# Optimization experiments

Measured on AMD Instinct MI355X. Metric: run time of the kernel, lower is better.

The kernel has to match this reference:

```python
import jax, jax.numpy as jnp
import numpy as np

IN, OUT, E, R = 2048, 2048, 8, 8

def setup_inputs() -> dict:
    key = jax.random.key(0)
    ks = jax.random.split(key, 8)
    B, S = 4, 2048
    x = jax.random.normal(ks[0], (B, S, IN), dtype=jnp.float32)
    routing_weights = jax.random.uniform(ks[1], (B, E), dtype=jnp.float32)
    W = jax.random.normal(ks[2], (OUT, IN), dtype=jnp.float32) / np.sqrt(IN).astype(np.float32)
    b = jax.random.normal(ks[3], (OUT,), dtype=jnp.float32) * 0.01
    lora_A_s = jax.random.normal(ks[4], (IN, R), dtype=jnp.float32) / np.sqrt(IN).astype(np.float32)
    lora_B_s = jax.random.normal(ks[5], (R, OUT), dtype=jnp.float32) * 0.01
    lora_A_e = jax.random.normal(ks[6], (E, IN, R), dtype=jnp.float32) / np.sqrt(IN).astype(np.float32)
    lora_B_e = jax.random.normal(ks[7], (E, R, OUT), dtype=jnp.float32) * 0.01
    return {"x": x, "routing_weights": routing_weights, "W": W, "b": b,
            "lora_A_s": lora_A_s, "lora_B_s": lora_B_s,
            "lora_A_e": lora_A_e, "lora_B_e": lora_B_e}

def reference(x, routing_weights, W, b, lora_A_s, lora_B_s, lora_A_e, lora_B_e):
    # base linear: [B,S,IN] @ [IN,OUT] + [OUT]
    base_out = jnp.einsum('bsi,oi->bso', x, W) + b
    # shared low-rank path
    shared_out = (x @ lora_A_s) @ lora_B_s
    # all experts batched: t[b,s,e,r] = x @ A_e[e]; weighted reduce over experts
    t = jnp.einsum('bsi,eir->bser', x, lora_A_e)          # [B,S,E,R]
    expert_out = jnp.einsum('bser,ero,be->bso', t, lora_B_e, routing_weights)
    return base_out + shared_out + expert_out
```

## Files before the change

### kernel.cpp

```cpp
#include <hip/hip_runtime.h>
#include <hip/hip_bf16.h>

#define IN_DIM 2048
#define OUT_DIM 2048
#define NE 8
#define M_TOT 8192
#define RANK_PAD 128
#define K_EXT 2176
#define NKT 34

typedef short short8 __attribute__((ext_vector_type(8)));
typedef float floatx4 __attribute__((ext_vector_type(4)));
typedef unsigned short us;

__device__ __forceinline__ us f2bf(float f) {
    __hip_bfloat16 h = __float2bfloat16(f);
    return *reinterpret_cast<us*>(&h);
}

__device__ __forceinline__ void gld_lds16(const void* g, void* l) {
    __builtin_amdgcn_global_load_lds(
        (const __attribute__((address_space(1))) void*)g,
        (__attribute__((address_space(3))) void*)l, 16, 0, 0);
}


__device__ __forceinline__ void stage2(const us* src, char* lds) {
    gld_lds16(src, lds);
    gld_lds16(src + 128 * K_EXT, lds + 8192);
}

__device__ __forceinline__ void mfma_quad(floatx4 (&acc)[8][4], const short8 (&af)[4],
                                          const short8 (&bf)[4], int mq) {
#pragma unroll
    for (int i = 0; i < 4; ++i)
#pragma unroll
        for (int ni = 0; ni < 4; ++ni)
            acc[mq * 4 + i][ni] =
                __builtin_amdgcn_mfma_f32_16x16x32_bf16(af[i], bf[ni], acc[mq * 4 + i][ni], 0, 0, 0);
}

template <int SM, int VM0, int VM2, bool RD3>
__device__ __forceinline__ void ktile(
    const us* __restrict__ pA, const us* __restrict__ pB, int k1, int k2,
    const char* smC, const char* smN, char* lwC, char* lwN,
    int ab, int bb,
    short8 (&afA)[4], short8 (&afB)[4], short8 (&bfA)[4], short8 (&bfB)[4],
    floatx4 (&acc)[8][4])
{
#pragma unroll
    for (int i = 0; i < 4; ++i) afB[i] = *(const short8*)(smC + ab + (4 + i) * 1024);
    asm volatile("s_waitcnt lgkmcnt(4)" ::: "memory");
    __builtin_amdgcn_sched_barrier(0);
    __builtin_amdgcn_s_setprio(1);
    mfma_quad(acc, afA, bfA, 0);
    __builtin_amdgcn_s_setprio(0);
    if (SM & 1) stage2(pA + k1 + 32, lwN + 32768);
    if (VM0 == 8)      asm volatile("s_waitcnt vmcnt(8)" ::: "memory");
    else if (VM0 == 0) asm volatile("s_waitcnt vmcnt(0)" ::: "memory");
    __builtin_amdgcn_s_barrier();

#pragma unroll
    for (int i = 0; i < 4; ++i) afA[i] = *(const short8*)(smC + 32768 + ab + (4 + i) * 1024);
#pragma unroll
    for (int i = 0; i < 4; ++i) bfB[i] = *(const short8*)(smC + 32768 + bb + i * 1024);
    asm volatile("s_waitcnt lgkmcnt(8)" ::: "memory");
    __builtin_amdgcn_sched_barrier(0);
    __builtin_amdgcn_s_setprio(1);
    mfma_quad(acc, afB, bfA, 1);
    __builtin_amdgcn_s_setprio(0);
    if (SM & 2) stage2(pB + k2, lwC + 16384);
    __builtin_amdgcn_s_barrier();

#pragma unroll
    for (int i = 0; i < 4; ++i) afB[i] = *(const short8*)(smC + 32768 + ab + i * 1024);
    asm volatile("s_waitcnt lgkmcnt(4)" ::: "memory");
    __builtin_amdgcn_sched_barrier(0);
    __builtin_amdgcn_s_setprio(1);
    mfma_quad(acc, afA, bfB, 1);
    __builtin_amdgcn_s_setprio(0);
    if (SM & 4) stage2(pA + k2, lwC);
    if (VM2 == 8)      asm volatile("s_waitcnt vmcnt(8)" ::: "memory");
    else if (VM2 == 4) asm volatile("s_waitcnt vmcnt(4)" ::: "memory");
    __builtin_amdgcn_s_barrier();

    if (RD3) {
#pragma unroll
        for (int i = 0; i < 4; ++i) afA[i] = *(const short8*)(smN + ab + i * 1024);
#pragma unroll
        for (int i = 0; i < 4; ++i) bfA[i] = *(const short8*)(smN + bb + i * 1024);
        asm volatile("s_waitcnt lgkmcnt(8)" ::: "memory");
    } else {
        asm volatile("s_waitcnt lgkmcnt(0)" ::: "memory");
    }
    __builtin_amdgcn_sched_barrier(0);
    __builtin_amdgcn_s_setprio(1);
    mfma_quad(acc, afB, bfB, 0);
    __builtin_amdgcn_s_setprio(0);
    if (SM & 8) stage2(pB + k2 + 32, lwC + 49152);
    __builtin_amdgcn_s_barrier();
}

__global__ __launch_bounds__(512) void main_gemm8(const us* __restrict__ A,
                                                  const us* __restrict__ B,
                                                  const float* __restrict__ bias,
                                                  float* __restrict__ out) {
    extern __shared__ char smem[];
    int tid = threadIdx.x;
    int lane = tid & 63, w = tid >> 6;
    int wm = w >> 2, wn = w & 3;
    int rlo = lane & 15, kq = lane >> 4;

    int b = blockIdx.x;
    int bs = (b & 7) * 32 + (b >> 3);
    int m0 = (bs >> 3) * 256, n0 = (bs & 7) * 256;

    int swz = (kq ^ ((rlo >> 1) & 3)) * 16;
    int ab = (wm * 128 + rlo) * 64 + swz;
    int bb = 16384 + (wn * 64 + rlo) * 64 + swz;

    int r0 = tid >> 2;
    int ps = tid & 3;
    int ssw = (ps ^ ((r0 >> 1) & 3)) * 8;
    const us* pA = A + (size_t)(m0 + r0) * K_EXT + ssw;
    const us* pB = B + (size_t)(n0 + r0) * K_EXT + ssw;
    char* lw0 = smem + w * 1024;
    char* lw1 = lw0 + 65536;
    const char* sm0 = smem;
    const char* sm1 = smem + 65536;

    floatx4 acc[8][4];
#pragma unroll
    for (int mi = 0; mi < 8; ++mi)
#pragma unroll
        for (int ni = 0; ni < 4; ++ni) acc[mi][ni] = (floatx4)0.f;

    stage2(pA,      lw0);
    stage2(pB,      lw0 + 16384);
    stage2(pA + 32, lw0 + 32768);
    stage2(pB + 32, lw0 + 49152);
    stage2(pA + 64, lw1);
    stage2(pB + 64, lw1 + 16384);
    stage2(pB + 96, lw1 + 49152);
    asm volatile("s_waitcnt vmcnt(10)" ::: "memory");
    __builtin_amdgcn_s_barrier();

    short8 afA[4], afB[4], bfA[4], bfB[4];
#pragma unroll
    for (int i = 0; i < 4; ++i) afA[i] = *(const short8*)(sm0 + ab + i * 1024);
#pragma unroll
    for (int i = 0; i < 4; ++i) bfA[i] = *(const short8*)(sm0 + bb + i * 1024);

    for (int tt = 0; tt < 16; ++tt) {
        int t0 = tt * 2;
        ktile<0xF, 8, 8, true>(pA, pB, (t0 + 1) * 64, (t0 + 2) * 64,
                               sm0, sm1, lw0, lw1, ab, bb, afA, afB, bfA, bfB, acc);
        ktile<0xF, 8, 8, true>(pA, pB, (t0 + 2) * 64, (t0 + 3) * 64,
                               sm1, sm0, lw1, lw0, ab, bb, afA, afB, bfA, bfB, acc);
    }
    ktile<0x1, 8, 4, true>(pA, pB, 33 * 64, 34 * 64,
                           sm0, sm1, lw0, lw1, ab, bb, afA, afB, bfA, bfB, acc);
    ktile<0x0, 0, -1, false>(pA, pB, 0, 0,
                             sm1, sm0, lw1, lw0, ab, bb, afA, afB, bfA, bfB, acc);

    float bbias[4];
#pragma unroll
    for (int ni = 0; ni < 4; ++ni) bbias[ni] = bias[n0 + wn * 64 + ni * 16 + rlo];
#pragma unroll
    for (int mi = 0; mi < 8; ++mi) {
        int row = m0 + wm * 128 + mi * 16 + kq * 4;
#pragma unroll
        for (int ni = 0; ni < 4; ++ni) {
            int col = n0 + wn * 64 + ni * 16 + rlo;
#pragma unroll
            for (int r = 0; r < 4; ++r)
                out[(size_t)(row + r) * OUT_DIM + col] = acc[mi][ni][r] + bbias[ni];
        }
    }
}

__global__ void prep_wb(const float* __restrict__ W, const float* __restrict__ Bs,
                        const float* __restrict__ Be, const float* __restrict__ As,
                        const float* __restrict__ Ae, us* __restrict__ Bext,
                        us* __restrict__ AcatT) {
    int blk = blockIdx.x;
    int t = threadIdx.x;
    if (blk < OUT_DIM) {
        int n = blk;
        const float4* src = (const float4*)(W + (size_t)n * IN_DIM + t * 8);
        float4 v0 = src[0], v1 = src[1];
        short8 o;
        o[0] = (short)f2bf(v0.x); o[1] = (short)f2bf(v0.y); o[2] = (short)f2bf(v0.z); o[3] = (short)f2bf(v0.w);
        o[4] = (short)f2bf(v1.x); o[5] = (short)f2bf(v1.y); o[6] = (short)f2bf(v1.z); o[7] = (short)f2bf(v1.w);
        *(short8*)(Bext + (size_t)n * K_EXT + t * 8) = o;
        if (t < RANK_PAD) {
            float v = 0.f;
            if (t < 8)       v = Bs[(size_t)t * OUT_DIM + n];
            else if (t < 72) v = Be[(size_t)(t - 8) * OUT_DIM + n];
            Bext[(size_t)n * K_EXT + IN_DIM + t] = f2bf(v);
        }
    } else {
        int kp = blk - OUT_DIM;
        int i0 = t * 8;
        short8 o;
#pragma unroll
        for (int j = 0; j < 8; ++j) {
            int i = i0 + j;
            float v = 0.f;
            if (kp < 8)       v = As[(size_t)i * 8 + kp];
            else if (kp < 72) v = Ae[(size_t)((kp - 8) >> 3) * IN_DIM * 8 + (size_t)i * 8 + ((kp - 8) & 7)];
            o[j] = (short)f2bf(v);
        }
        *(short8*)(AcatT + (size_t)kp * IN_DIM + i0) = o;
    }
}

__global__ __launch_bounds__(512) void tgemm_fused(const float* __restrict__ x,
                                                   us* __restrict__ Aext,
                                                   const us* __restrict__ AcatT,
                                                   const float* __restrict__ routing) {
    __shared__ floatx4 red[8][64][6];
    int tid = threadIdx.x;
    int lane = tid & 63, w = tid >> 6;
    int rlo = lane & 15, kq = lane >> 4;
    int mbase = blockIdx.x * 16;

    floatx4 acc[6];
#pragma unroll
    for (int ni = 0; ni < 6; ++ni) acc[ni] = (floatx4)0.f;

    const float* xrow = x + (size_t)(mbase + rlo) * IN_DIM + w * 256 + kq * 8;
    us* arow = Aext + (size_t)(mbase + rlo) * K_EXT + w * 256 + kq * 8;
    const us* bbase = AcatT + (size_t)rlo * IN_DIM + w * 256 + kq * 8;

#pragma unroll
    for (int kt = 0; kt < 8; ++kt) {
        int k0 = kt * 32;
        float4 v0 = *(const float4*)(xrow + k0);
        float4 v1 = *(const float4*)(xrow + k0 + 4);
        short8 a;
        a[0] = (short)f2bf(v0.x); a[1] = (short)f2bf(v0.y); a[2] = (short)f2bf(v0.z); a[3] = (short)f2bf(v0.w);
        a[4] = (short)f2bf(v1.x); a[5] = (short)f2bf(v1.y); a[6] = (short)f2bf(v1.z); a[7] = (short)f2bf(v1.w);
        *(short8*)(arow + k0) = a;
#pragma unroll
        for (int ni = 0; ni < 6; ++ni) {
            short8 bfr = *(const short8*)(bbase + (size_t)(ni * 16) * IN_DIM + k0);
            acc[ni] = __builtin_amdgcn_mfma_f32_16x16x32_bf16(a, bfr, acc[ni], 0, 0, 0);
        }
    }

#pragma unroll
    for (int ni = 0; ni < 6; ++ni) red[w][lane][ni] = acc[ni];
    __syncthreads();
    if (w == 0) {
#pragma unroll
        for (int ni = 0; ni < 6; ++ni) {
            floatx4 s = red[0][lane][ni];
#pragma unroll
            for (int ww = 1; ww < 8; ++ww) s += red[ww][lane][ni];
            int col = ni * 16 + rlo;
#pragma unroll
            for (int r = 0; r < 4; ++r) {
                int row = mbase + kq * 4 + r;
                float fac = (col < 8) ? 1.f
                          : (col < 72 ? routing[(row >> 11) * NE + ((col - 8) >> 3)] : 0.f);
                Aext[(size_t)row * K_EXT + IN_DIM + col] = f2bf(s[r] * fac);
            }
        }
#pragma unroll
        for (int c = 0; c < 2; ++c) {
            int col = 96 + c * 16 + rlo;
#pragma unroll
            for (int r = 0; r < 4; ++r)
                Aext[(size_t)(mbase + kq * 4 + r) * K_EXT + IN_DIM + col] = 0;
        }
    }
}

extern "C" void kernel_launch(void* const* d_in, const int* in_sizes, int n_in,
                              void* d_out, int out_size, void* d_ws, size_t ws_size,
                              hipStream_t stream) {
    const float* x   = (const float*)d_in[0];
    const float* rw  = (const float*)d_in[1];
    const float* W   = (const float*)d_in[2];
    const float* bv  = (const float*)d_in[3];
    const float* As  = (const float*)d_in[4];
    const float* Bs  = (const float*)d_in[5];
    const float* Ae  = (const float*)d_in[6];
    const float* Be  = (const float*)d_in[7];
    float* out = (float*)d_out;

    size_t offA = 0;
    size_t offB = offA + (size_t)M_TOT * K_EXT * sizeof(us);
    size_t offC = offB + (size_t)OUT_DIM * K_EXT * sizeof(us);
    size_t need = offC + (size_t)96 * IN_DIM * sizeof(us);
    if (ws_size < need) return;

    us* Aext  = (us*)((char*)d_ws + offA);
    us* Bext  = (us*)((char*)d_ws + offB);
    us* AcatT = (us*)((char*)d_ws + offC);

    hipFuncSetAttribute((const void*)main_gemm8,
                        hipFuncAttributeMaxDynamicSharedMemorySize, 131072);

    prep_wb<<<OUT_DIM + 96, 256, 0, stream>>>(W, Bs, Be, As, Ae, Bext, AcatT);
    tgemm_fused<<<M_TOT / 16, 512, 0, stream>>>(x, Aext, AcatT, rw);
    main_gemm8<<<256, 512, 131072, stream>>>(Aext, Bext, bv, out);
}
```

Measured before the change: 114.6 us.

## Fuse prep, low-rank projection and main GEMM into one cooperative kernel

Merges the three kernel launches (weight/activation conversion, the LoRA projection GEMM, and the main bf16 GEMM) into a single cooperative kernel of 256 blocks separated by two grid-wide syncs. This removes launch gaps and tail effects between kernels. The x-to-bf16 conversion moves into the prep phase, so the projection phase rereads bf16 Aext instead of fp32 x, and each block now handles 32 rows instead of 16. In exchange, the prep and projection phases run on only 256 blocks of 512 threads held to the main GEMM's large shared-memory footprint, which limits their parallelism, and the grid syncs add overhead.

Measured after the change: 344.3 us. +200.5%, slower.

```diff
diff --git a/kernel.cpp b/kernel.cpp
--- a/kernel.cpp
+++ b/kernel.cpp
@@ -1,5 +1,8 @@
 #include <hip/hip_runtime.h>
 #include <hip/hip_bf16.h>
+#include <hip/hip_cooperative_groups.h>
+
+namespace cg = cooperative_groups;
 
 #define IN_DIM 2048
 #define OUT_DIM 2048
@@ -7,7 +10,6 @@
 #define M_TOT 8192
 #define RANK_PAD 128
 #define K_EXT 2176
-#define NKT 34
 
 typedef short short8 __attribute__((ext_vector_type(8)));
 typedef float floatx4 __attribute__((ext_vector_type(4)));
@@ -16,6 +18,15 @@
 __device__ __forceinline__ us f2bf(float f) {
     __hip_bfloat16 h = __float2bfloat16(f);
     return *reinterpret_cast<us*>(&h);
+}
+
+__device__ __forceinline__ short8 cvt8(float4 v0, float4 v1) {
+    short8 o;
+    o[0] = (short)f2bf(v0.x); o[1] = (short)f2bf(v0.y);
+    o[2] = (short)f2bf(v0.z); o[3] = (short)f2bf(v0.w);
+    o[4] = (short)f2bf(v1.x); o[5] = (short)f2bf(v1.y);
+    o[6] = (short)f2bf(v1.z); o[7] = (short)f2bf(v1.w);
+    return o;
 }
 
 __device__ __forceinline__ void gld_lds16(const void* g, void* l) {
@@ -101,18 +112,14 @@
     __builtin_amdgcn_s_barrier();
 }
 
-__global__ __launch_bounds__(512) void main_gemm8(const us* __restrict__ A,
-                                                  const us* __restrict__ B,
-                                                  const float* __restrict__ bias,
-                                                  float* __restrict__ out) {
-    extern __shared__ char smem[];
-    int tid = threadIdx.x;
+__device__ void run_main_gemm(char* smem, int tid, int bid,
+                              const us* __restrict__ A, const us* __restrict__ B,
+                              const float* __restrict__ bias, float* __restrict__ out) {
     int lane = tid & 63, w = tid >> 6;
     int wm = w >> 2, wn = w & 3;
     int rlo = lane & 15, kq = lane >> 4;
 
-    int b = blockIdx.x;
-    int bs = (b & 7) * 32 + (b >> 3);
+    int bs = (bid & 7) * 32 + (bid >> 3);
     int m0 = (bs >> 3) * 256, n0 = (bs & 7) * 256;
 
     int swz = (kq ^ ((rlo >> 1) & 3)) * 16;
@@ -179,102 +186,131 @@
     }
 }
 
-__global__ void prep_wb(const float* __restrict__ W, const float* __restrict__ Bs,
-                        const float* __restrict__ Be, const float* __restrict__ As,
-                        const float* __restrict__ Ae, us* __restrict__ Bext,
-                        us* __restrict__ AcatT) {
-    int blk = blockIdx.x;
-    int t = threadIdx.x;
-    if (blk < OUT_DIM) {
-        int n = blk;
-        const float4* src = (const float4*)(W + (size_t)n * IN_DIM + t * 8);
-        float4 v0 = src[0], v1 = src[1];
-        short8 o;
-        o[0] = (short)f2bf(v0.x); o[1] = (short)f2bf(v0.y); o[2] = (short)f2bf(v0.z); o[3] = (short)f2bf(v0.w);
-        o[4] = (short)f2bf(v1.x); o[5] = (short)f2bf(v1.y); o[6] = (short)f2bf(v1.z); o[7] = (short)f2bf(v1.w);
-        *(short8*)(Bext + (size_t)n * K_EXT + t * 8) = o;
-        if (t < RANK_PAD) {
+__global__ __launch_bounds__(512) void fused_all(
+    const float* __restrict__ x, const float* __restrict__ routing,
+    const float* __restrict__ W, const float* __restrict__ bias,
+    const float* __restrict__ As, const float* __restrict__ Bs,
+    const float* __restrict__ Ae, const float* __restrict__ Be,
+    float* __restrict__ out, us* __restrict__ Aext, us* __restrict__ Bext,
+    us* __restrict__ AcatT)
+{
+    extern __shared__ char smem[];
+    int tid = threadIdx.x;
+    int bid = blockIdx.x;
+
+    {
+        int half = tid >> 8;
+        int t = tid & 255;
+        int col = t * 8;
+#pragma unroll 4
+        for (int rr = 0; rr < 16; ++rr) {
+            int row = bid * 32 + rr * 2 + half;
+            const float4* src = (const float4*)(x + (size_t)row * IN_DIM + col);
+            *(short8*)(Aext + (size_t)row * K_EXT + col) = cvt8(src[0], src[1]);
+        }
+#pragma unroll
+        for (int rr = 0; rr < 4; ++rr) {
+            int n = bid * 8 + rr * 2 + half;
+            const float4* src = (const float4*)(W + (size_t)n * IN_DIM + col);
+            *(short8*)(Bext + (size_t)n * K_EXT + col) = cvt8(src[0], src[1]);
+        }
+#pragma unroll
+        for (int it = 0; it < 2; ++it) {
+            int q = it * 512 + tid;
+            int rrow = q >> 7, ccol = q & 127;
+            int n = bid * 8 + rrow;
             float v = 0.f;
-            if (t < 8)       v = Bs[(size_t)t * OUT_DIM + n];
-            else if (t < 72) v = Be[(size_t)(t - 8) * OUT_DIM + n];
-            Bext[(size_t)n * K_EXT + IN_DIM + t] = f2bf(v);
-        }
-    } else {
-        int kp = blk - OUT_DIM;
-        int i0 = t * 8;
-        short8 o;
-#pragma unroll
-        for (int j = 0; j < 8; ++j) {
-            int i = i0 + j;
-            float v = 0.f;
-            if (kp < 8)       v = As[(size_t)i * 8 + kp];
-            else if (kp < 72) v = Ae[(size_t)((kp - 8) >> 3) * IN_DIM * 8 + (size_t)i * 8 + ((kp - 8) & 7)];
-            o[j] = (short)f2bf(v);
-        }
-        *(short8*)(AcatT + (size_t)kp * IN_DIM + i0) = o;
-    }
-}
-
-__global__ __launch_bounds__(512) void tgemm_fused(const float* __restrict__ x,
-                                                   us* __restrict__ Aext,
-                                                   const us* __restrict__ AcatT,
-                                                   const float* __restrict__ routing) {
-    __shared__ floatx4 red[8][64][6];
-    int tid = threadIdx.x;
-    int lane = tid & 63, w = tid >> 6;
-    int rlo = lane & 15, kq = lane >> 4;
-    int mbase = blockIdx.x * 16;
-
-    floatx4 acc[6];
-#pragma unroll
-    for (int ni = 0; ni < 6; ++ni) acc[ni] = (floatx4)0.f;
-
-    const float* xrow = x + (size_t)(mbase + rlo) * IN_DIM + w * 256 + kq * 8;
-    us* arow = Aext + (size_t)(mbase + rlo) * K_EXT + w * 256 + kq * 8;
-    const us* bbase = AcatT + (size_t)rlo * IN_DIM + w * 256 + kq * 8;
-
-#pragma unroll
-    for (int kt = 0; kt < 8; ++kt) {
-        int k0 = kt * 32;
-        float4 v0 = *(const float4*)(xrow + k0);
-        float4 v1 = *(const float4*)(xrow + k0 + 4);
-        short8 a;
-        a[0] = (short)f2bf(v0.x); a[1] = (short)f2bf(v0.y); a[2] = (short)f2bf(v0.z); a[3] = (short)f2bf(v0.w);
-        a[4] = (short)f2bf(v1.x); a[5] = (short)f2bf(v1.y); a[6] = (short)f2bf(v1.z); a[7] = (short)f2bf(v1.w);
-        *(short8*)(arow + k0) = a;
-#pragma unroll
-        for (int ni = 0; ni < 6; ++ni) {
-            short8 bfr = *(const short8*)(bbase + (size_t)(ni * 16) * IN_DIM + k0);
-            acc[ni] = __builtin_amdgcn_mfma_f32_16x16x32_bf16(a, bfr, acc[ni], 0, 0, 0);
-        }
-    }
-
-#pragma unroll
-    for (int ni = 0; ni < 6; ++ni) red[w][lane][ni] = acc[ni];
-    __syncthreads();
-    if (w == 0) {
-#pragma unroll
-        for (int ni = 0; ni < 6; ++ni) {
-            floatx4 s = red[0][lane][ni];
-#pragma unroll
-            for (int ww = 1; ww < 8; ++ww) s += red[ww][lane][ni];
-            int col = ni * 16 + rlo;
-#pragma unroll
-            for (int r = 0; r < 4; ++r) {
-                int row = mbase + kq * 4 + r;
-                float fac = (col < 8) ? 1.f
-                          : (col < 72 ? routing[(row >> 11) * NE + ((col - 8) >> 3)] : 0.f);
-                Aext[(size_t)row * K_EXT + IN_DIM + col] = f2bf(s[r] * fac);
+            if (ccol < 8)       v = Bs[(size_t)ccol * OUT_DIM + n];
+            else if (ccol < 72) v = Be[(size_t)(ccol - 8) * OUT_DIM + n];
+            Bext[(size_t)n * K_EXT + IN_DIM + ccol] = f2bf(v);
+        }
+        if (bid < 96) {
+            int kp = bid;
+            int i0 = tid * 4;
+#pragma unroll
+            for (int j = 0; j < 4; ++j) {
+                int i = i0 + j;
+                float v = 0.f;
+                if (kp < 8)       v = As[(size_t)i * 8 + kp];
+                else if (kp < 72) v = Ae[(size_t)(kp - 8) + (size_t)i * 8
+                                         + (size_t)((kp - 8) >> 3) * (IN_DIM * 8 - 8)
+                                         + (size_t)0];
+                AcatT[(size_t)kp * IN_DIM + i] = f2bf(v);
             }
         }
-#pragma unroll
-        for (int c = 0; c < 2; ++c) {
-            int col = 96 + c * 16 + rlo;
-#pragma unroll
-            for (int r = 0; r < 4; ++r)
-                Aext[(size_t)(mbase + kq * 4 + r) * K_EXT + IN_DIM + col] = 0;
-        }
-    }
+    }
+
+    cg::grid_group grid = cg::this_grid();
+    __threadfence();
+    grid.sync();
+    __threadfence();
+
+    {
+        floatx4* red = (floatx4*)smem;
+        int lane = tid & 63, w = tid >> 6;
+        int rlo = lane & 15, kq = lane >> 4;
+        int mbase = bid * 32;
+
+        floatx4 acc[2][6];
+#pragma unroll
+        for (int rg = 0; rg < 2; ++rg)
+#pragma unroll
+            for (int ni = 0; ni < 6; ++ni) acc[rg][ni] = (floatx4)0.f;
+
+        const us* a0p = Aext + (size_t)(mbase + rlo) * K_EXT + w * 256 + kq * 8;
+        const us* a1p = Aext + (size_t)(mbase + 16 + rlo) * K_EXT + w * 256 + kq * 8;
+        const us* b0p = AcatT + (size_t)rlo * IN_DIM + w * 256 + kq * 8;
+
+#pragma unroll
+        for (int kt = 0; kt < 8; ++kt) {
+            int k0 = kt * 32;
+            short8 a0 = *(const short8*)(a0p + k0);
+            short8 a1 = *(const short8*)(a1p + k0);
+#pragma unroll
+            for (int ni = 0; ni < 6; ++ni) {
+                short8 bfr = *(const short8*)(b0p + (size_t)(ni * 16) * IN_DIM + k0);
+                acc[0][ni] = __builtin_amdgcn_mfma_f32_16x16x32_bf16(a0, bfr, acc[0][ni], 0, 0, 0);
+                acc[1][ni] = __builtin_amdgcn_mfma_f32_16x16x32_bf16(a1, bfr, acc[1][ni], 0, 0, 0);
+            }
+        }
+#pragma unroll
+        for (int rg = 0; rg < 2; ++rg)
+#pragma unroll
+            for (int ni = 0; ni < 6; ++ni)
+                red[(w * 64 + lane) * 12 + rg * 6 + ni] = acc[rg][ni];
+        __syncthreads();
+        if (w < 2) {
+            int rg = w;
+#pragma unroll
+            for (int ni = 0; ni < 6; ++ni) {
+                floatx4 s = red[lane * 12 + rg * 6 + ni];
+#pragma unroll
+                for (int ww = 1; ww < 8; ++ww)
+                    s += red[(ww * 64 + lane) * 12 + rg * 6 + ni];
+                int col = ni * 16 + rlo;
+#pragma unroll
+                for (int r = 0; r < 4; ++r) {
+                    int row = mbase + rg * 16 + kq * 4 + r;
+                    float fac = (col < 8) ? 1.f
+                              : (col < 72 ? routing[(row >> 11) * NE + ((col - 8) >> 3)] : 0.f);
+                    Aext[(size_t)row * K_EXT + IN_DIM + col] = f2bf(s[r] * fac);
+                }
+            }
+#pragma unroll
+            for (int c = 0; c < 2; ++c) {
+                int col = 96 + c * 16 + rlo;
+#pragma unroll
+                for (int r = 0; r < 4; ++r)
+                    Aext[(size_t)(mbase + rg * 16 + kq * 4 + r) * K_EXT + IN_DIM + col] = 0;
+            }
+        }
+    }
+
+    __threadfence();
+    grid.sync();
+    __threadfence();
+
+    run_main_gemm(smem, tid, bid, Aext, Bext, bias, out);
 }
 
 extern "C" void kernel_launch(void* const* d_in, const int* in_sizes, int n_in,
@@ -300,10 +336,12 @@
     us* Bext  = (us*)((char*)d_ws + offB);
     us* AcatT = (us*)((char*)d_ws + offC);
 
-    hipFuncSetAttribute((const void*)main_gemm8,
+    hipFuncSetAttribute((const void*)fused_all,
                         hipFuncAttributeMaxDynamicSharedMemorySize, 131072);
 
-    prep_wb<<<OUT_DIM + 96, 256, 0, stream>>>(W, Bs, Be, As, Ae, Bext, AcatT);
-    tgemm_fused<<<M_TOT / 16, 512, 0, stream>>>(x, Aext, AcatT, rw);
-    main_gemm8<<<256, 512, 131072, stream>>>(Aext, Bext, bv, out);
-}
+    void* args[] = {(void*)&x, (void*)&rw, (void*)&W, (void*)&bv,
+                    (void*)&As, (void*)&Bs, (void*)&Ae, (void*)&Be,
+                    (void*)&out, (void*)&Aext, (void*)&Bext, (void*)&AcatT};
+    hipLaunchCooperativeKernel((void*)fused_all, dim3(256), dim3(512),
+                               args, 131072, stream);
+}
```

## Merge W-to-bf16 conversion into the x-projection kernel as extra blocks

Applied to the files above, without the earlier changes.

The weight conversion (W and the LoRA B matrices into the extended bf16 B operand) moves out of the first prep kernel and runs as 512 extra blocks of the x-cast/LoRA-A projection kernel. Only the small A-matrix transpose stays in a separate tiny kernel. This lets the weight cast run alongside the activation work and shortens the serial chain of prep launches. The cost is one more small launch and blocks that each carry the large shared-memory reduction buffer even when they do no reduction.

Result: no change. 115.1 us (+0.4%).

```diff
diff --git a/kernel.cpp b/kernel.cpp
--- a/kernel.cpp
+++ b/kernel.cpp
@@ -7,8 +7,8 @@
 #define M_TOT 8192
 #define RANK_PAD 128
 #define K_EXT 2176
-#define NKT 34
-
+
+typedef short short4v __attribute__((ext_vector_type(4)));
 typedef short short8 __attribute__((ext_vector_type(8)));
 typedef float floatx4 __attribute__((ext_vector_type(4)));
 typedef unsigned short us;
@@ -179,51 +179,61 @@
     }
 }
 
-__global__ void prep_wb(const float* __restrict__ W, const float* __restrict__ Bs,
-                        const float* __restrict__ Be, const float* __restrict__ As,
-                        const float* __restrict__ Ae, us* __restrict__ Bext,
-                        us* __restrict__ AcatT) {
-    int blk = blockIdx.x;
-    int t = threadIdx.x;
-    if (blk < OUT_DIM) {
-        int n = blk;
-        const float4* src = (const float4*)(W + (size_t)n * IN_DIM + t * 8);
-        float4 v0 = src[0], v1 = src[1];
-        short8 o;
-        o[0] = (short)f2bf(v0.x); o[1] = (short)f2bf(v0.y); o[2] = (short)f2bf(v0.z); o[3] = (short)f2bf(v0.w);
-        o[4] = (short)f2bf(v1.x); o[5] = (short)f2bf(v1.y); o[6] = (short)f2bf(v1.z); o[7] = (short)f2bf(v1.w);
-        *(short8*)(Bext + (size_t)n * K_EXT + t * 8) = o;
-        if (t < RANK_PAD) {
-            float v = 0.f;
-            if (t < 8)       v = Bs[(size_t)t * OUT_DIM + n];
-            else if (t < 72) v = Be[(size_t)(t - 8) * OUT_DIM + n];
-            Bext[(size_t)n * K_EXT + IN_DIM + t] = f2bf(v);
-        }
-    } else {
-        int kp = blk - OUT_DIM;
-        int i0 = t * 8;
-        short8 o;
-#pragma unroll
-        for (int j = 0; j < 8; ++j) {
-            int i = i0 + j;
-            float v = 0.f;
-            if (kp < 8)       v = As[(size_t)i * 8 + kp];
-            else if (kp < 72) v = Ae[(size_t)((kp - 8) >> 3) * IN_DIM * 8 + (size_t)i * 8 + ((kp - 8) & 7)];
-            o[j] = (short)f2bf(v);
-        }
-        *(short8*)(AcatT + (size_t)kp * IN_DIM + i0) = o;
-    }
-}
-
-__global__ __launch_bounds__(512) void tgemm_fused(const float* __restrict__ x,
-                                                   us* __restrict__ Aext,
-                                                   const us* __restrict__ AcatT,
-                                                   const float* __restrict__ routing) {
+__global__ void prep_acat(const float* __restrict__ As, const float* __restrict__ Ae,
+                          us* __restrict__ AcatT) {
+    int kp = blockIdx.x;
+    int i0 = threadIdx.x * 8;
+    short8 o;
+#pragma unroll
+    for (int j = 0; j < 8; ++j) {
+        int i = i0 + j;
+        float v = 0.f;
+        if (kp < 8)       v = As[(size_t)i * 8 + kp];
+        else if (kp < 72) v = Ae[(size_t)((kp - 8) >> 3) * IN_DIM * 8 + (size_t)i * 8 + ((kp - 8) & 7)];
+        o[j] = (short)f2bf(v);
+    }
+    *(short8*)(AcatT + (size_t)kp * IN_DIM + i0) = o;
+}
+
+__global__ __launch_bounds__(512) void prep_tgemm(
+    const float* __restrict__ x, us* __restrict__ Aext,
+    const us* __restrict__ AcatT, const float* __restrict__ routing,
+    const float* __restrict__ W, const float* __restrict__ Bs,
+    const float* __restrict__ Be, us* __restrict__ Bext)
+{
     __shared__ floatx4 red[8][64][6];
     int tid = threadIdx.x;
+    int bid = blockIdx.x;
+
+    if (bid >= 512) {
+        int base = (bid - 512) * 4;
+        int half = tid >> 8;
+        int t = tid & 255;
+        int col = t * 8;
+#pragma unroll
+        for (int rr = 0; rr < 2; ++rr) {
+            int n = base + rr * 2 + half;
+            const float4* src = (const float4*)(W + (size_t)n * IN_DIM + col);
+            float4 v0 = src[0], v1 = src[1];
+            short8 o;
+            o[0] = (short)f2bf(v0.x); o[1] = (short)f2bf(v0.y);
+            o[2] = (short)f2bf(v0.z); o[3] = (short)f2bf(v0.w);
+            o[4] = (short)f2bf(v1.x); o[5] = (short)f2bf(v1.y);
+            o[6] = (short)f2bf(v1.z); o[7] = (short)f2bf(v1.w);
+            *(short8*)(Bext + (size_t)n * K_EXT + col) = o;
+        }
+        int rrow = tid >> 7, ccol = tid & 127;
+        int n = base + rrow;
+        float v = 0.f;
+        if (ccol < 8)       v = Bs[(size_t)ccol * OUT_DIM + n];
+        else if (ccol < 72) v = Be[(size_t)(ccol - 8) * OUT_DIM + n];
+        Bext[(size_t)n * K_EXT + IN_DIM + ccol] = f2bf(v);
+        return;
+    }
+
     int lane = tid & 63, w = tid >> 6;
     int rlo = lane & 15, kq = lane >> 4;
-    int mbase = blockIdx.x * 16;
+    int mbase = bid * 16;
 
     floatx4 acc[6];
 #pragma unroll
@@ -239,8 +249,10 @@
         float4 v0 = *(const float4*)(xrow + k0);
         float4 v1 = *(const float4*)(xrow + k0 + 4);
         short8 a;
-        a[0] = (short)f2bf(v0.x); a[1] = (short)f2bf(v0.y); a[2] = (short)f2bf(v0.z); a[3] = (short)f2bf(v0.w);
-        a[4] = (short)f2bf(v1.x); a[5] = (short)f2bf(v1.y); a[6] = (short)f2bf(v1.z); a[7] = (short)f2bf(v1.w);
+        a[0] = (short)f2bf(v0.x); a[1] = (short)f2bf(v0.y);
+        a[2] = (short)f2bf(v0.z); a[3] = (short)f2bf(v0.w);
+        a[4] = (short)f2bf(v1.x); a[5] = (short)f2bf(v1.y);
+        a[6] = (short)f2bf(v1.z); a[7] = (short)f2bf(v1.w);
         *(short8*)(arow + k0) = a;
 #pragma unroll
         for (int ni = 0; ni < 6; ++ni) {
@@ -303,7 +315,7 @@
     hipFuncSetAttribute((const void*)main_gemm8,
                         hipFuncAttributeMaxDynamicSharedMemorySize, 131072);
 
-    prep_wb<<<OUT_DIM + 96, 256, 0, stream>>>(W, Bs, Be, As, Ae, Bext, AcatT);
-    tgemm_fused<<<M_TOT / 16, 512, 0, stream>>>(x, Aext, AcatT, rw);
+    prep_acat<<<96, 256, 0, stream>>>(As, Ae, AcatT);
+    prep_tgemm<<<1024, 512, 0, stream>>>(x, Aext, AcatT, rw, W, Bs, Be, Bext);
     main_gemm8<<<256, 512, 131072, stream>>>(Aext, Bext, bv, out);
 }
```

## Move x bf16 conversion into combined streaming prep kernel and read bf16 in tgemm

Applied to the files above, without the earlier changes.

The fp32-to-bf16 conversion of x moves out of the low-rank projection kernel into a single prep kernel that also converts W and builds the LoRA B/A extension tables, with more work per 512-thread block. The projection kernel then reads the already-converted bf16 activations instead of fp32 x. The intent is to decouple bandwidth-bound conversion from the MFMA reduction kernel and make conversion a pure coalesced stream. The cost is an extra read of the bf16 activation buffer in the projection kernel, and the B-extension and A-transpose parts now use narrower scalar stores.

New measurement: 119.4 us. 1.04x slower.

```diff
diff --git a/kernel.cpp b/kernel.cpp
--- a/kernel.cpp
+++ b/kernel.cpp
@@ -7,7 +7,6 @@
 #define M_TOT 8192
 #define RANK_PAD 128
 #define K_EXT 2176
-#define NKT 34
 
 typedef short short8 __attribute__((ext_vector_type(8)));
 typedef float floatx4 __attribute__((ext_vector_type(4)));
@@ -16,6 +15,15 @@
 __device__ __forceinline__ us f2bf(float f) {
     __hip_bfloat16 h = __float2bfloat16(f);
     return *reinterpret_cast<us*>(&h);
+}
+
+__device__ __forceinline__ short8 cvt8(float4 v0, float4 v1) {
+    short8 o;
+    o[0] = (short)f2bf(v0.x); o[1] = (short)f2bf(v0.y);
+    o[2] = (short)f2bf(v0.z); o[3] = (short)f2bf(v0.w);
+    o[4] = (short)f2bf(v1.x); o[5] = (short)f2bf(v1.y);
+    o[6] = (short)f2bf(v1.z); o[7] = (short)f2bf(v1.w);
+    return o;
 }
 
 __device__ __forceinline__ void gld_lds16(const void* g, void* l) {
@@ -179,46 +187,61 @@
     }
 }
 
-__global__ void prep_wb(const float* __restrict__ W, const float* __restrict__ Bs,
-                        const float* __restrict__ Be, const float* __restrict__ As,
-                        const float* __restrict__ Ae, us* __restrict__ Bext,
-                        us* __restrict__ AcatT) {
-    int blk = blockIdx.x;
-    int t = threadIdx.x;
-    if (blk < OUT_DIM) {
-        int n = blk;
-        const float4* src = (const float4*)(W + (size_t)n * IN_DIM + t * 8);
-        float4 v0 = src[0], v1 = src[1];
-        short8 o;
-        o[0] = (short)f2bf(v0.x); o[1] = (short)f2bf(v0.y); o[2] = (short)f2bf(v0.z); o[3] = (short)f2bf(v0.w);
-        o[4] = (short)f2bf(v1.x); o[5] = (short)f2bf(v1.y); o[6] = (short)f2bf(v1.z); o[7] = (short)f2bf(v1.w);
-        *(short8*)(Bext + (size_t)n * K_EXT + t * 8) = o;
-        if (t < RANK_PAD) {
+__global__ __launch_bounds__(512) void prep_stream(
+    const float* __restrict__ x, const float* __restrict__ W,
+    const float* __restrict__ Bs, const float* __restrict__ Be,
+    const float* __restrict__ As, const float* __restrict__ Ae,
+    us* __restrict__ Aext, us* __restrict__ Bext, us* __restrict__ AcatT)
+{
+    int bid = blockIdx.x;
+    int tid = threadIdx.x;
+
+    if (bid < 512) {
+        int half = tid >> 8;
+        int col = (tid & 255) * 8;
+#pragma unroll 8
+        for (int pass = 0; pass < 8; ++pass) {
+            int row = bid * 16 + pass * 2 + half;
+            const float4* src = (const float4*)(x + (size_t)row * IN_DIM + col);
+            *(short8*)(Aext + (size_t)row * K_EXT + col) = cvt8(src[0], src[1]);
+        }
+    } else if (bid < 640) {
+        int half = tid >> 8;
+        int col = (tid & 255) * 8;
+#pragma unroll 8
+        for (int pass = 0; pass < 8; ++pass) {
+            int n = (bid - 512) * 16 + pass * 2 + half;
+            const float4* src = (const float4*)(W + (size_t)n * IN_DIM + col);
+            *(short8*)(Bext + (size_t)n * K_EXT + col) = cvt8(src[0], src[1]);
+        }
+    } else if (bid < 704) {
+        int n = (bid - 640) * 32 + (tid >> 4);
+        int c0 = (tid & 15) * 8;
+#pragma unroll 8
+        for (int j = 0; j < 8; ++j) {
+            int c = c0 + j;
             float v = 0.f;
-            if (t < 8)       v = Bs[(size_t)t * OUT_DIM + n];
-            else if (t < 72) v = Be[(size_t)(t - 8) * OUT_DIM + n];
-            Bext[(size_t)n * K_EXT + IN_DIM + t] = f2bf(v);
+            if (c < 8)       v = Bs[(size_t)c * OUT_DIM + n];
+            else if (c < 72) v = Be[(size_t)(c - 8) * OUT_DIM + n];
+            Bext[(size_t)n * K_EXT + IN_DIM + c] = f2bf(v);
         }
     } else {
-        int kp = blk - OUT_DIM;
-        int i0 = t * 8;
-        short8 o;
-#pragma unroll
-        for (int j = 0; j < 8; ++j) {
+        int kp = bid - 704;
+        int i0 = tid * 4;
+#pragma unroll 4
+        for (int j = 0; j < 4; ++j) {
             int i = i0 + j;
             float v = 0.f;
             if (kp < 8)       v = As[(size_t)i * 8 + kp];
             else if (kp < 72) v = Ae[(size_t)((kp - 8) >> 3) * IN_DIM * 8 + (size_t)i * 8 + ((kp - 8) & 7)];
-            o[j] = (short)f2bf(v);
-        }
-        *(short8*)(AcatT + (size_t)kp * IN_DIM + i0) = o;
-    }
-}
-
-__global__ __launch_bounds__(512) void tgemm_fused(const float* __restrict__ x,
-                                                   us* __restrict__ Aext,
-                                                   const us* __restrict__ AcatT,
-                                                   const float* __restrict__ routing) {
+            AcatT[(size_t)kp * IN_DIM + i] = f2bf(v);
+        }
+    }
+}
+
+__global__ __launch_bounds__(512) void tgemm_bf(us* __restrict__ Aext,
+                                                const us* __restrict__ AcatT,
+                                                const float* __restrict__ routing) {
     __shared__ floatx4 red[8][64][6];
     int tid = threadIdx.x;
     int lane = tid & 63, w = tid >> 6;
@@ -229,19 +252,13 @@
 #pragma unroll
     for (int ni = 0; ni < 6; ++ni) acc[ni] = (floatx4)0.f;
 
-    const float* xrow = x + (size_t)(mbase + rlo) * IN_DIM + w * 256 + kq * 8;
-    us* arow = Aext + (size_t)(mbase + rlo) * K_EXT + w * 256 + kq * 8;
+    const us* arow = Aext + (size_t)(mbase + rlo) * K_EXT + w * 256 + kq * 8;
     const us* bbase = AcatT + (size_t)rlo * IN_DIM + w * 256 + kq * 8;
 
 #pragma unroll
     for (int kt = 0; kt < 8; ++kt) {
         int k0 = kt * 32;
-        float4 v0 = *(const float4*)(xrow + k0);
-        float4 v1 = *(const float4*)(xrow + k0 + 4);
-        short8 a;
-        a[0] = (short)f2bf(v0.x); a[1] = (short)f2bf(v0.y); a[2] = (short)f2bf(v0.z); a[3] = (short)f2bf(v0.w);
-        a[4] = (short)f2bf(v1.x); a[5] = (short)f2bf(v1.y); a[6] = (short)f2bf(v1.z); a[7] = (short)f2bf(v1.w);
-        *(short8*)(arow + k0) = a;
+        short8 a = *(const short8*)(arow + k0);
 #pragma unroll
         for (int ni = 0; ni < 6; ++ni) {
             short8 bfr = *(const short8*)(bbase + (size_t)(ni * 16) * IN_DIM + k0);
@@ -303,7 +320,7 @@
     hipFuncSetAttribute((const void*)main_gemm8,
                         hipFuncAttributeMaxDynamicSharedMemorySize, 131072);
 
-    prep_wb<<<OUT_DIM + 96, 256, 0, stream>>>(W, Bs, Be, As, Ae, Bext, AcatT);
-    tgemm_fused<<<M_TOT / 16, 512, 0, stream>>>(x, Aext, AcatT, rw);
+    prep_stream<<<800, 512, 0, stream>>>(x, W, Bs, Be, As, Ae, Aext, Bext, AcatT);
+    tgemm_bf<<<512, 512, 0, stream>>>(Aext, AcatT, rw);
     main_gemm8<<<256, 512, 131072, stream>>>(Aext, Bext, bv, out);
 }
```
